# Kernel tuning notes

Hardware: AMD Instinct MI355X
Metric: run time of the kernel (lower is better)

## Reference

```python
import jax, jax.numpy as jnp
import numpy as np

HEADS = 8
DIM_HEAD = 64
DIM = 512
LN_EPS = 1e-5


def rotate_half(t):
    shp = t.shape
    t = t.reshape(*shp[:-1], -1, 2)
    t1, t2 = t[..., 0], t[..., 1]
    return jnp.stack((-t2, t1), axis=-1).reshape(shp)


def apply_rope(freqs, t):
    # freqs: (b,1,n,dh) broadcast against t: (b,h,n,dh); rot_dim == dh so no pass-through
    return t * jnp.cos(freqs) + rotate_half(t) * jnp.sin(freqs)


def layer_norm(x, g, b, eps=LN_EPS):
    mu = jnp.mean(x, axis=-1, keepdims=True)
    var = jnp.var(x, axis=-1, keepdims=True)
    return (x - mu) * jax.lax.rsqrt(var + eps) * g + b


def setup_inputs() -> dict:
    key = jax.random.key(0)
    ks = jax.random.split(key, 8)
    n, b = 2048, 4
    inner = HEADS * DIM_HEAD
    inp = {
        "x": jax.random.normal(ks[0], (n, b, DIM), dtype=jnp.float32),
        "rot_pos_emb": jax.random.uniform(ks[1], (b, n, DIM_HEAD), dtype=jnp.float32),
        "Wq": jax.random.normal(ks[2], (inner, DIM), dtype=jnp.float32) * (DIM ** -0.5),
        "Wk": jax.random.normal(ks[3], (inner, DIM), dtype=jnp.float32) * (DIM ** -0.5),
        "Wv": jax.random.normal(ks[4], (inner, DIM), dtype=jnp.float32) * (DIM ** -0.5),
        "Wo": jax.random.normal(ks[5], (DIM, inner), dtype=jnp.float32) * (inner ** -0.5),
        "bo": jnp.zeros((DIM,), dtype=jnp.float32),
        "ln_g": jnp.ones((DIM,), dtype=jnp.float32),
        "ln_b": jnp.zeros((DIM,), dtype=jnp.float32),
        "head_scale": jnp.ones((1, HEADS, 1, 1), dtype=jnp.float32),
        "ls_scale": jnp.full((1, 1, DIM), 1e-5, dtype=jnp.float32),
    }
    return inp


def reference(x, rot_pos_emb, Wq, Wk, Wv, Wo, bo, ln_g, ln_b, head_scale, ls_scale):
    n, b, d = x.shape
    h, dh = HEADS, DIM_HEAD
    scale = dh ** -0.5

    xb = jnp.transpose(x, (1, 0, 2))  # (b,n,d)
    q = (xb @ Wq.T).reshape(b, n, h, dh).transpose(0, 2, 1, 3)  # (b,h,n,dh)
    k = (xb @ Wk.T).reshape(b, n, h, dh).transpose(0, 2, 1, 3)
    v = (xb @ Wv.T).reshape(b, n, h, dh).transpose(0, 2, 1, 3)

    freqs = rot_pos_emb[:, None]  # (b,1,n,dh)
    q = apply_rope(freqs, q)
    k = apply_rope(freqs, k)

    sim = jnp.einsum("bhid,bhjd->bhij", q, k) * scale
    mask = jnp.triu(jnp.ones((n, n), dtype=bool), 1)
    sim = jnp.where(mask[None, None], -jnp.finfo(sim.dtype).max, sim)
    attn = jax.nn.softmax(sim, axis=-1)

    out = jnp.einsum("bhij,bhjd->bhid", attn, v) * head_scale
    out = out.transpose(0, 2, 1, 3).reshape(b, n, h * dh)
    out = layer_norm(out @ Wo.T + bo, ln_g, ln_b)
    out = jnp.transpose(out, (1, 0, 2))  # (n,b,d)
    return ls_scale * out
```

## Files before the change

kernel.cpp:

```cpp
#include <hip/hip_runtime.h>
#include <hip/hip_bf16.h>
#include <math.h>

#define NSEQ 2048
#define NB 4
#define NH 8
#define DH 64
#define DMODEL 512
#define MROWS (NSEQ * 4)

typedef short bf16x8 __attribute__((ext_vector_type(8)));
typedef float f32x4 __attribute__((ext_vector_type(4)));

static __device__ __forceinline__ short f2bf_r(float f) {
    unsigned u = __float_as_uint(f);
    u += 0x7FFF + ((u >> 16) & 1);
    return (short)(u >> 16);
}
static __device__ __forceinline__ unsigned bfpack(float a, float b) {
    unsigned ua = __float_as_uint(a); ua += 0x7FFF + ((ua >> 16) & 1);
    unsigned ub = __float_as_uint(b); ub += 0x7FFF + ((ub >> 16) & 1);
    return (ua >> 16) | (ub & 0xFFFF0000u);
}

__global__ __launch_bounds__(256) void k0_convert(
    const float* __restrict__ x, const float* __restrict__ Wq,
    const float* __restrict__ Wk, const float* __restrict__ Wv,
    const float* __restrict__ Wo,
    __hip_bfloat16* __restrict__ xb, __hip_bfloat16* __restrict__ Wb)
{
    const int idx = blockIdx.x * 256 + threadIdx.x;
    if (idx < 8192 * 128) {
        const int row = idx >> 7, c = (idx & 127) << 2;
        const int bi = row >> 11, ni = row & 2047;
        float4 v = *(const float4*)(x + ((size_t)(ni * NB + bi)) * DMODEL + c);
        uint2 u; u.x = bfpack(v.x, v.y); u.y = bfpack(v.z, v.w);
        *(uint2*)((short*)xb + (size_t)row * 512 + c) = u;
    } else {
        const int j = idx - 8192 * 128;
        const int row = j >> 7, c = (j & 127) << 2;
        const float* src = (row < 512) ? Wq : (row < 1024) ? Wk
                         : (row < 1536) ? Wv : Wo;
        const int rr = row & 511;
        float4 v = *(const float4*)(src + (size_t)rr * 512 + c);
        uint2 u; u.x = bfpack(v.x, v.y); u.y = bfpack(v.z, v.w);
        *(uint2*)((short*)Wb + (size_t)row * 512 + c) = u;
    }
}

__global__ __launch_bounds__(256) void k1_qkv(
    const __hip_bfloat16* __restrict__ xb, const float* __restrict__ rope,
    const __hip_bfloat16* __restrict__ Wb,
    __hip_bfloat16* __restrict__ Qs, __hip_bfloat16* __restrict__ Ks,
    __hip_bfloat16* __restrict__ Vs)
{
    __shared__ short As[128 * 72];
    __shared__ short Bs[128 * 72];
    const int t = threadIdx.x;
    const int w = t >> 6, L = t & 63, lo = L & 15, g = L >> 4;
    const int mh = (w >> 1) << 6, nh = (w & 1) << 6;

    const int lid = (int)(blockIdx.y * gridDim.x + blockIdx.x);
    const int xcd = lid & 7, slot = lid >> 3;
    const int row_blk = xcd * 8 + (slot & 7);
    const int col_blk = slot >> 3;
    const int row0 = row_blk * 128, col0 = col_blk * 128;

    f32x4 acc[4][4] = {};
    for (int k0 = 0; k0 < DMODEL; k0 += 64) {
        __syncthreads();
#pragma unroll
        for (int c = 0; c < 4; ++c) {
            const int idx = c * 256 + t;
            const int m = idx >> 3, kb = idx & 7;
            *(uint4*)&As[m * 72 + kb * 8] =
                *(const uint4*)((const short*)xb + (size_t)(row0 + m) * 512 + k0 + kb * 8);
            *(uint4*)&Bs[m * 72 + kb * 8] =
                *(const uint4*)((const short*)Wb + (size_t)(col0 + m) * 512 + k0 + kb * 8);
        }
        __syncthreads();
#pragma unroll
        for (int ks = 0; ks < 2; ++ks) {
            bf16x8 af[4], bfr[4];
#pragma unroll
            for (int mi = 0; mi < 4; ++mi)
                af[mi] = *(const bf16x8*)&As[(mh + mi * 16 + lo) * 72 + ks * 32 + g * 8];
#pragma unroll
            for (int ni = 0; ni < 4; ++ni)
                bfr[ni] = *(const bf16x8*)&Bs[(nh + ni * 16 + lo) * 72 + ks * 32 + g * 8];
#pragma unroll
            for (int mi = 0; mi < 4; ++mi)
#pragma unroll
                for (int ni = 0; ni < 4; ++ni)
                    acc[mi][ni] = __builtin_amdgcn_mfma_f32_16x16x32_bf16(
                        af[mi], bfr[ni], acc[mi][ni], 0, 0, 0);
        }
    }

    const int region = col0 >> 9;
    const int cbase = col0 & 511;
    const int bi = row0 >> 11;
    const int ni0 = row0 & 2047;
    const float SC = 0.125f * 1.44269504088896f;
    if (region < 2) {
        short* outp = (short*)((region == 0) ? Qs : Ks);
        const float qs = (region == 0) ? SC : 1.0f;
#pragma unroll
        for (int ni = 0; ni < 4; ++ni) {
            const int c = cbase + nh + ni * 16 + lo;
            const int h = c >> 6, e = c & 63;
            const float sgn = (e & 1) ? 1.0f : -1.0f;
            short* hb = outp + ((size_t)(bi * NH + h) * 128) * 1024
                        + (e >> 5) * 512 + ((e >> 3) & 3) * 16 * 8 + (e & 7);
#pragma unroll
            for (int mi = 0; mi < 4; ++mi) {
#pragma unroll
                for (int r = 0; r < 4; ++r) {
                    const int nseq = ni0 + mh + mi * 16 + g * 4 + r;
                    const float f = rope[((size_t)bi * NSEQ + nseq) * DH + e];
                    const float v = acc[mi][ni][r];
                    const float p = __shfl_xor(v, 1);
                    float sv, cv;
                    __sincosf(f, &sv, &cv);
                    const float rv = (v * cv + sgn * p * sv) * qs;
                    hb[(size_t)(nseq >> 4) * 1024 + (nseq & 15) * 8] = f2bf_r(rv);
                }
            }
        }
    } else {
#pragma unroll
        for (int ni = 0; ni < 4; ++ni) {
            const int c = cbase + nh + ni * 16 + lo;
            const int h = c >> 6, e = c & 63;
            short* hb = (short*)Vs + ((size_t)(bi * NH + h) * 256) * 512
                        + (e >> 4) * 512 + (e & 15) * 8;
#pragma unroll
            for (int mi = 0; mi < 4; ++mi) {
                const int nb = ni0 + mh + mi * 16 + g * 4;
                uint2 u;
                u.x = bfpack(acc[mi][ni][0], acc[mi][ni][1]);
                u.y = bfpack(acc[mi][ni][2], acc[mi][ni][3]);
                *(uint2*)(hb + (size_t)(nb >> 5) * 2048 + ((nb >> 3) & 3) * 16 * 8
                          + (nb & 7)) = u;
            }
        }
    }
}

__global__ __launch_bounds__(256, 3) void k2_attn(
    const __hip_bfloat16* __restrict__ Qs, const __hip_bfloat16* __restrict__ Ks,
    const __hip_bfloat16* __restrict__ Vs, const float* __restrict__ head_scale,
    __hip_bfloat16* __restrict__ Ob)
{
    __shared__ short sP[4][16 * 72];

    const int t = threadIdx.x;
    const int w = t >> 6, L = t & 63, lo = L & 15, g = L >> 4;

    const int lid = (int)blockIdx.x;
    const int xcd = lid & 7, slot = lid >> 3;
    const int bh = xcd * 4 + (slot & 3);
    const int qb = 31 - (slot >> 2);
    const int qt = qb * 4 + w;
    const int bi = bh >> 3, h = bh & 7;

    const short* Kp = (const short*)Ks + (size_t)bh * (128 * 1024) + L * 8;
    const short* Vp = (const short*)Vs + (size_t)bh * (256 * 512) + L * 8;
    const short* Qp = (const short*)Qs + (size_t)bh * (128 * 1024)
                      + (size_t)qt * 1024 + L * 8;
    const bf16x8 qf0 = *(const bf16x8*)(Qp);
    const bf16x8 qf1 = *(const bf16x8*)(Qp + 512);

    f32x4 acc[4] = {};
    float l_i = 0.f;
    const int nkt = qb + 1;

    auto body = [&](const bf16x8* kc0, const bf16x8* kc1, int kt) {
        const bool diag = (kt == qb);
        const int mlim = diag ? w : 3;
        const bool hi = (mlim >= 2);

        bf16x8 vb0[4], vb1[4];
        const short* vp0 = Vp + (size_t)(kt * 8) * 512;
#pragma unroll
        for (int dt = 0; dt < 4; ++dt) {
            vb0[dt] = *(const bf16x8*)(vp0 + dt * 512);
            if (hi) vb1[dt] = *(const bf16x8*)(vp0 + (4 + dt) * 512);
        }

        f32x4 s[4];
#pragma unroll
        for (int mt = 0; mt < 4; ++mt) {
            if (mt <= mlim) {
                f32x4 z = {};
                z = __builtin_amdgcn_mfma_f32_16x16x32_bf16(kc0[mt], qf0, z, 0, 0, 0);
                s[mt] = __builtin_amdgcn_mfma_f32_16x16x32_bf16(kc1[mt], qf1, z, 0, 0, 0);
                if (diag && mt == mlim) {
#pragma unroll
                    for (int r = 0; r < 4; ++r)
                        if ((g * 4 + r) > lo) s[mt][r] = -1e30f;
                }
            }
        }

#pragma unroll
        for (int mt = 0; mt < 4; ++mt) {
            uint2 u;
            if (mt <= mlim) {
                const float p0 = exp2f(s[mt][0] - 16.f);
                const float p1 = exp2f(s[mt][1] - 16.f);
                const float p2 = exp2f(s[mt][2] - 16.f);
                const float p3 = exp2f(s[mt][3] - 16.f);
                l_i += (p0 + p1) + (p2 + p3);
                u.x = bfpack(p0, p1); u.y = bfpack(p2, p3);
            } else {
                u.x = 0u; u.y = 0u;
            }
            *(uint2*)&sP[w][lo * 72 + mt * 16 + g * 4] = u;
        }

        const bf16x8 pb0 = *(const bf16x8*)&sP[w][lo * 72 + g * 8];
        if (hi) {
            const bf16x8 pb1 = *(const bf16x8*)&sP[w][lo * 72 + 32 + g * 8];
#pragma unroll
            for (int dt = 0; dt < 4; ++dt) {
                acc[dt] = __builtin_amdgcn_mfma_f32_16x16x32_bf16(vb0[dt], pb0, acc[dt], 0, 0, 0);
                acc[dt] = __builtin_amdgcn_mfma_f32_16x16x32_bf16(vb1[dt], pb1, acc[dt], 0, 0, 0);
            }
        } else {
#pragma unroll
            for (int dt = 0; dt < 4; ++dt)
                acc[dt] = __builtin_amdgcn_mfma_f32_16x16x32_bf16(vb0[dt], pb0, acc[dt], 0, 0, 0);
        }
    };

    bf16x8 kA0[4], kA1[4], kB0[4], kB1[4];
#pragma unroll
    for (int mt = 0; mt < 4; ++mt) {
        const short* kp = Kp + (size_t)mt * 1024;
        kA0[mt] = *(const bf16x8*)kp;
        kA1[mt] = *(const bf16x8*)(kp + 512);
    }
    int kt = 0;
#pragma unroll 1
    while (true) {
        if (kt + 1 < nkt) {
            const short* kp = Kp + (size_t)((kt + 1) * 4) * 1024;
#pragma unroll
            for (int mt = 0; mt < 4; ++mt) {
                kB0[mt] = *(const bf16x8*)(kp + mt * 1024);
                kB1[mt] = *(const bf16x8*)(kp + mt * 1024 + 512);
            }
        }
        body(kA0, kA1, kt);
        ++kt;
        if (kt >= nkt) break;
        if (kt + 1 < nkt) {
            const short* kp = Kp + (size_t)((kt + 1) * 4) * 1024;
#pragma unroll
            for (int mt = 0; mt < 4; ++mt) {
                kA0[mt] = *(const bf16x8*)(kp + mt * 1024);
                kA1[mt] = *(const bf16x8*)(kp + mt * 1024 + 512);
            }
        }
        body(kB0, kB1, kt);
        ++kt;
        if (kt >= nkt) break;
    }

    l_i += __shfl_xor(l_i, 16);
    l_i += __shfl_xor(l_i, 32);
    const float f = head_scale[h] / l_i;
    const int q = qt * 16 + lo;
    short* op = (short*)Ob + ((size_t)bi * NSEQ + q) * DMODEL + h * DH + g * 4;
#pragma unroll
    for (int dt = 0; dt < 4; ++dt) {
        uint2 u;
        u.x = bfpack(acc[dt][0] * f, acc[dt][1] * f);
        u.y = bfpack(acc[dt][2] * f, acc[dt][3] * f);
        *(uint2*)(op + dt * 16) = u;
    }
}

__global__ __launch_bounds__(256) void k3_proj(
    const __hip_bfloat16* __restrict__ Ob, const __hip_bfloat16* __restrict__ Wob,
    const float* __restrict__ bo, float* __restrict__ C2)
{
    __shared__ short As[128 * 72];
    __shared__ short Bs[128 * 72];
    const int t = threadIdx.x;
    const int w = t >> 6, L = t & 63, lo = L & 15, g = L >> 4;
    const int mh = (w >> 1) << 6, nh = (w & 1) << 6;

    const int lid = (int)(blockIdx.y * gridDim.x + blockIdx.x);
    const int xcd = lid & 7, slot = lid >> 3;
    const int row_blk = xcd * 8 + (slot & 7);
    const int col_blk = slot >> 3;
    const int row0 = row_blk * 128, col0 = col_blk * 128;

    f32x4 acc[4][4] = {};
    for (int k0 = 0; k0 < DMODEL; k0 += 64) {
        __syncthreads();
#pragma unroll
        for (int c = 0; c < 4; ++c) {
            const int idx = c * 256 + t;
            const int m = idx >> 3, kb = idx & 7;
            *(uint4*)&As[m * 72 + kb * 8] =
                *(const uint4*)((const short*)Ob + (size_t)(row0 + m) * 512 + k0 + kb * 8);
            *(uint4*)&Bs[m * 72 + kb * 8] =
                *(const uint4*)((const short*)Wob + (size_t)(col0 + m) * 512 + k0 + kb * 8);
        }
        __syncthreads();
#pragma unroll
        for (int ks = 0; ks < 2; ++ks) {
            bf16x8 af[4], bfr[4];
#pragma unroll
            for (int mi = 0; mi < 4; ++mi)
                af[mi] = *(const bf16x8*)&As[(mh + mi * 16 + lo) * 72 + ks * 32 + g * 8];
#pragma unroll
            for (int ni = 0; ni < 4; ++ni)
                bfr[ni] = *(const bf16x8*)&Bs[(nh + ni * 16 + lo) * 72 + ks * 32 + g * 8];
#pragma unroll
            for (int mi = 0; mi < 4; ++mi)
#pragma unroll
                for (int ni = 0; ni < 4; ++ni)
                    acc[mi][ni] = __builtin_amdgcn_mfma_f32_16x16x32_bf16(
                        af[mi], bfr[ni], acc[mi][ni], 0, 0, 0);
        }
    }
#pragma unroll
    for (int ni = 0; ni < 4; ++ni) {
        const int c = col0 + nh + ni * 16 + lo;
        const float b = bo[c];
#pragma unroll
        for (int mi = 0; mi < 4; ++mi) {
#pragma unroll
            for (int r = 0; r < 4; ++r) {
                const int m = row0 + mh + mi * 16 + g * 4 + r;
                C2[(size_t)m * DMODEL + c] = acc[mi][ni][r] + b;
            }
        }
    }
}

__global__ __launch_bounds__(256) void k4_ln(
    const float* __restrict__ C2, const float* __restrict__ g,
    const float* __restrict__ bln, const float* __restrict__ ls,
    float* __restrict__ out)
{
    const int m = blockIdx.x;
    const int bi = m >> 11, ni = m & (NSEQ - 1);
    const float* row = C2 + (size_t)m * DMODEL;
    const int t = threadIdx.x;
    float v0 = row[t], v1 = row[t + 256];
    float s = v0 + v1, sq2 = v0 * v0 + v1 * v1;
#pragma unroll
    for (int off = 32; off > 0; off >>= 1) {
        s += __shfl_down(s, off);
        sq2 += __shfl_down(sq2, off);
    }
    __shared__ float red[8];
    const int wid = t >> 6;
    if ((t & 63) == 0) { red[wid] = s; red[wid + 4] = sq2; }
    __syncthreads();
    s = red[0] + red[1] + red[2] + red[3];
    sq2 = red[4] + red[5] + red[6] + red[7];
    const float mean = s * (1.f / 512.f);
    const float var = sq2 * (1.f / 512.f) - mean * mean;
    const float rstd = rsqrtf(var + 1e-5f);
    float* ob = out + ((size_t)ni * NB + bi) * DMODEL;
    ob[t]       = ((v0 - mean) * rstd * g[t]       + bln[t])       * ls[t];
    ob[t + 256] = ((v1 - mean) * rstd * g[t + 256] + bln[t + 256]) * ls[t + 256];
}

extern "C" void kernel_launch(void* const* d_in, const int* in_sizes, int n_in,
                              void* d_out, int out_size, void* d_ws, size_t ws_size,
                              hipStream_t stream) {
    const float* x          = (const float*)d_in[0];
    const float* rope       = (const float*)d_in[1];
    const float* Wq         = (const float*)d_in[2];
    const float* Wk         = (const float*)d_in[3];
    const float* Wv         = (const float*)d_in[4];
    const float* Wo         = (const float*)d_in[5];
    const float* bo         = (const float*)d_in[6];
    const float* ln_g       = (const float*)d_in[7];
    const float* ln_b       = (const float*)d_in[8];
    const float* head_scale = (const float*)d_in[9];
    const float* ls_scale   = (const float*)d_in[10];
    float* out = (float*)d_out;

    char* wsb = (char*)d_ws;
    __hip_bfloat16* xb  = (__hip_bfloat16*)(wsb);
    __hip_bfloat16* Wb  = (__hip_bfloat16*)(wsb + ((size_t) 8 << 20));
    __hip_bfloat16* Qs  = (__hip_bfloat16*)(wsb + ((size_t)10 << 20));
    __hip_bfloat16* Ks  = (__hip_bfloat16*)(wsb + ((size_t)18 << 20));
    __hip_bfloat16* Vs  = (__hip_bfloat16*)(wsb + ((size_t)26 << 20));
    __hip_bfloat16* Ob  = (__hip_bfloat16*)(wsb + ((size_t)34 << 20));
    float*          C2  = (float*)(wsb + ((size_t)10 << 20));
    __hip_bfloat16* Wob = Wb + (size_t)1536 * 512;

    k0_convert<<<5120, 256, 0, stream>>>(x, Wq, Wk, Wv, Wo, xb, Wb);
    k1_qkv<<<dim3(64, 12), 256, 0, stream>>>(xb, rope, Wb, Qs, Ks, Vs);
    k2_attn<<<1024, 256, 0, stream>>>(Qs, Ks, Vs, head_scale, Ob);
    k3_proj<<<dim3(64, 4), 256, 0, stream>>>(Ob, Wob, bo, C2);
    k4_ln<<<MROWS, 256, 0, stream>>>(C2, ln_g, ln_b, ls_scale, out);
}
```

Baseline: 188.4 us.

## Precompute RoPE sin/cos and swap QK GEMM operands for vectorized epilogue

RoPE cos/sin tables are now computed once in the conversion kernel instead of per element inside the QKV epilogue. The QKV GEMM is split into a Q/K kernel and a separate V kernel. The Q/K kernel swaps its MFMA operands so each lane holds four consecutive head-dim values, which lets the rotation pair up inside a lane with no shuffle and write packed 8-byte stores. The goal is to remove the cross-lane shuffles, the repeated sincos calls and the scalar bf16 stores, at the cost of an extra kernel launch and 4 MB of cos/sin tables written and read back.

```diff
diff --git a/kernel.cpp b/kernel.cpp
--- a/kernel.cpp
+++ b/kernel.cpp
@@ -26,8 +26,9 @@
 __global__ __launch_bounds__(256) void k0_convert(
     const float* __restrict__ x, const float* __restrict__ Wq,
     const float* __restrict__ Wk, const float* __restrict__ Wv,
-    const float* __restrict__ Wo,
-    __hip_bfloat16* __restrict__ xb, __hip_bfloat16* __restrict__ Wb)
+    const float* __restrict__ Wo, const float* __restrict__ rope,
+    __hip_bfloat16* __restrict__ xb, __hip_bfloat16* __restrict__ Wb,
+    float* __restrict__ cs, float* __restrict__ sn)
 {
     const int idx = blockIdx.x * 256 + threadIdx.x;
     if (idx < 8192 * 128) {
@@ -36,7 +37,7 @@
         float4 v = *(const float4*)(x + ((size_t)(ni * NB + bi)) * DMODEL + c);
         uint2 u; u.x = bfpack(v.x, v.y); u.y = bfpack(v.z, v.w);
         *(uint2*)((short*)xb + (size_t)row * 512 + c) = u;
-    } else {
+    } else if (idx < 8192 * 128 + 2048 * 128) {
         const int j = idx - 8192 * 128;
         const int row = j >> 7, c = (j & 127) << 2;
         const float* src = (row < 512) ? Wq : (row < 1024) ? Wk
@@ -45,26 +46,37 @@
         float4 v = *(const float4*)(src + (size_t)rr * 512 + c);
         uint2 u; u.x = bfpack(v.x, v.y); u.y = bfpack(v.z, v.w);
         *(uint2*)((short*)Wb + (size_t)row * 512 + c) = u;
-    }
-}
-
-__global__ __launch_bounds__(256) void k1_qkv(
-    const __hip_bfloat16* __restrict__ xb, const float* __restrict__ rope,
-    const __hip_bfloat16* __restrict__ Wb,
-    __hip_bfloat16* __restrict__ Qs, __hip_bfloat16* __restrict__ Ks,
-    __hip_bfloat16* __restrict__ Vs)
+    } else {
+        const int j = idx - (8192 * 128 + 2048 * 128);
+        float4 f = *(const float4*)(rope + (size_t)j * 4);
+        float4 c4, s4;
+        __sincosf(f.x, &s4.x, &c4.x);
+        __sincosf(f.y, &s4.y, &c4.y);
+        __sincosf(f.z, &s4.z, &c4.z);
+        __sincosf(f.w, &s4.w, &c4.w);
+        *(float4*)(cs + (size_t)j * 4) = c4;
+        *(float4*)(sn + (size_t)j * 4) = s4;
+    }
+}
+
+__global__ __launch_bounds__(256) void k1_qk(
+    const __hip_bfloat16* __restrict__ xb, const float* __restrict__ cs,
+    const float* __restrict__ sn, const __hip_bfloat16* __restrict__ Wb,
+    __hip_bfloat16* __restrict__ Qs, __hip_bfloat16* __restrict__ Ks)
 {
     __shared__ short As[128 * 72];
     __shared__ short Bs[128 * 72];
     const int t = threadIdx.x;
     const int w = t >> 6, L = t & 63, lo = L & 15, g = L >> 4;
-    const int mh = (w >> 1) << 6, nh = (w & 1) << 6;
+    const int mhW = (w >> 1) << 6;
+    const int nhX = (w & 1) << 6;
 
     const int lid = (int)(blockIdx.y * gridDim.x + blockIdx.x);
     const int xcd = lid & 7, slot = lid >> 3;
     const int row_blk = xcd * 8 + (slot & 7);
     const int col_blk = slot >> 3;
     const int row0 = row_blk * 128, col0 = col_blk * 128;
+    const int bi = row0 >> 11, ni0 = row0 & 2047;
 
     f32x4 acc[4][4] = {};
     for (int k0 = 0; k0 < DMODEL; k0 += 64) {
@@ -84,10 +96,10 @@
             bf16x8 af[4], bfr[4];
 #pragma unroll
             for (int mi = 0; mi < 4; ++mi)
-                af[mi] = *(const bf16x8*)&As[(mh + mi * 16 + lo) * 72 + ks * 32 + g * 8];
+                af[mi] = *(const bf16x8*)&Bs[(mhW + mi * 16 + lo) * 72 + ks * 32 + g * 8];
 #pragma unroll
             for (int ni = 0; ni < 4; ++ni)
-                bfr[ni] = *(const bf16x8*)&Bs[(nh + ni * 16 + lo) * 72 + ks * 32 + g * 8];
+                bfr[ni] = *(const bf16x8*)&As[(nhX + ni * 16 + lo) * 72 + ks * 32 + g * 8];
 #pragma unroll
             for (int mi = 0; mi < 4; ++mi)
 #pragma unroll
@@ -97,52 +109,93 @@
         }
     }
 
-    const int region = col0 >> 9;
+    const float SC = 0.125f * 1.44269504088896f;
+    short* outp = (short*)((col0 < 512) ? Qs : Ks);
+    const float qs = (col0 < 512) ? SC : 1.0f;
     const int cbase = col0 & 511;
-    const int bi = row0 >> 11;
-    const int ni0 = row0 & 2047;
-    const float SC = 0.125f * 1.44269504088896f;
-    if (region < 2) {
-        short* outp = (short*)((region == 0) ? Qs : Ks);
-        const float qs = (region == 0) ? SC : 1.0f;
+#pragma unroll
+    for (int mi = 0; mi < 4; ++mi) {
+        const int c0 = cbase + mhW + mi * 16 + (g << 2);
+        const int h = c0 >> 6, e0 = c0 & 63;
+        short* hb = outp + ((size_t)(bi * NH + h)) * 131072
+                    + (e0 >> 5) * 512 + ((e0 >> 3) & 3) * 128 + (e0 & 7);
 #pragma unroll
         for (int ni = 0; ni < 4; ++ni) {
-            const int c = cbase + nh + ni * 16 + lo;
-            const int h = c >> 6, e = c & 63;
-            const float sgn = (e & 1) ? 1.0f : -1.0f;
-            short* hb = outp + ((size_t)(bi * NH + h) * 128) * 1024
-                        + (e >> 5) * 512 + ((e >> 3) & 3) * 16 * 8 + (e & 7);
-#pragma unroll
-            for (int mi = 0; mi < 4; ++mi) {
-#pragma unroll
-                for (int r = 0; r < 4; ++r) {
-                    const int nseq = ni0 + mh + mi * 16 + g * 4 + r;
-                    const float f = rope[((size_t)bi * NSEQ + nseq) * DH + e];
-                    const float v = acc[mi][ni][r];
-                    const float p = __shfl_xor(v, 1);
-                    float sv, cv;
-                    __sincosf(f, &sv, &cv);
-                    const float rv = (v * cv + sgn * p * sv) * qs;
-                    hb[(size_t)(nseq >> 4) * 1024 + (nseq & 15) * 8] = f2bf_r(rv);
-                }
-            }
-        }
-    } else {
-#pragma unroll
-        for (int ni = 0; ni < 4; ++ni) {
-            const int c = cbase + nh + ni * 16 + lo;
-            const int h = c >> 6, e = c & 63;
-            short* hb = (short*)Vs + ((size_t)(bi * NH + h) * 256) * 512
-                        + (e >> 4) * 512 + (e & 15) * 8;
-#pragma unroll
-            for (int mi = 0; mi < 4; ++mi) {
-                const int nb = ni0 + mh + mi * 16 + g * 4;
-                uint2 u;
-                u.x = bfpack(acc[mi][ni][0], acc[mi][ni][1]);
-                u.y = bfpack(acc[mi][ni][2], acc[mi][ni][3]);
-                *(uint2*)(hb + (size_t)(nb >> 5) * 2048 + ((nb >> 3) & 3) * 16 * 8
-                          + (nb & 7)) = u;
-            }
+            const int nseq = ni0 + nhX + ni * 16 + lo;
+            const float4 c4 = *(const float4*)(cs + ((size_t)bi * NSEQ + nseq) * DH + e0);
+            const float4 s4 = *(const float4*)(sn + ((size_t)bi * NSEQ + nseq) * DH + e0);
+            const f32x4 v = acc[mi][ni];
+            const float o0 = (v[0] * c4.x - v[1] * s4.x) * qs;
+            const float o1 = (v[1] * c4.y + v[0] * s4.y) * qs;
+            const float o2 = (v[2] * c4.z - v[3] * s4.z) * qs;
+            const float o3 = (v[3] * c4.w + v[2] * s4.w) * qs;
+            uint2 u; u.x = bfpack(o0, o1); u.y = bfpack(o2, o3);
+            *(uint2*)(hb + (size_t)(nseq >> 4) * 1024 + (nseq & 15) * 8) = u;
+        }
+    }
+}
+
+__global__ __launch_bounds__(256) void k1_v(
+    const __hip_bfloat16* __restrict__ xb, const __hip_bfloat16* __restrict__ Wb,
+    __hip_bfloat16* __restrict__ Vs)
+{
+    __shared__ short As[128 * 72];
+    __shared__ short Bs[128 * 72];
+    const int t = threadIdx.x;
+    const int w = t >> 6, L = t & 63, lo = L & 15, g = L >> 4;
+    const int mh = (w >> 1) << 6, nh = (w & 1) << 6;
+
+    const int lid = (int)(blockIdx.y * gridDim.x + blockIdx.x);
+    const int xcd = lid & 7, slot = lid >> 3;
+    const int row_blk = xcd * 8 + (slot & 7);
+    const int col_blk = slot >> 3;
+    const int row0 = row_blk * 128, col0 = col_blk * 128;
+    const int bi = row0 >> 11, ni0 = row0 & 2047;
+
+    f32x4 acc[4][4] = {};
+    for (int k0 = 0; k0 < DMODEL; k0 += 64) {
+        __syncthreads();
+#pragma unroll
+        for (int c = 0; c < 4; ++c) {
+            const int idx = c * 256 + t;
+            const int m = idx >> 3, kb = idx & 7;
+            *(uint4*)&As[m * 72 + kb * 8] =
+                *(const uint4*)((const short*)xb + (size_t)(row0 + m) * 512 + k0 + kb * 8);
+            *(uint4*)&Bs[m * 72 + kb * 8] =
+                *(const uint4*)((const short*)Wb + (size_t)(1024 + col0 + m) * 512 + k0 + kb * 8);
+        }
+        __syncthreads();
+#pragma unroll
+        for (int ks = 0; ks < 2; ++ks) {
+            bf16x8 af[4], bfr[4];
+#pragma unroll
+            for (int mi = 0; mi < 4; ++mi)
+                af[mi] = *(const bf16x8*)&As[(mh + mi * 16 + lo) * 72 + ks * 32 + g * 8];
+#pragma unroll
+            for (int ni = 0; ni < 4; ++ni)
+                bfr[ni] = *(const bf16x8*)&Bs[(nh + ni * 16 + lo) * 72 + ks * 32 + g * 8];
+#pragma unroll
+            for (int mi = 0; mi < 4; ++mi)
+#pragma unroll
+                for (int ni = 0; ni < 4; ++ni)
+                    acc[mi][ni] = __builtin_amdgcn_mfma_f32_16x16x32_bf16(
+                        af[mi], bfr[ni], acc[mi][ni], 0, 0, 0);
+        }
+    }
+#pragma unroll
+    for (int ni = 0; ni < 4; ++ni) {
+        const int c = col0 + nh + ni * 16 + lo;
+        const int h = c >> 6, e = c & 63;
+        short* hb = (short*)Vs + ((size_t)(bi * NH + h)) * 131072
+                    + (e >> 4) * 512 + (e & 15) * 8;
+#pragma unroll
+        for (int mi = 0; mi < 4; ++mi) {
+            const int nb = ni0 + mh + mi * 16 + g * 4;
+            uint2 u;
+            u.x = bfpack(acc[mi][ni][0], acc[mi][ni][1]);
+            u.y = bfpack(acc[mi][ni][2], acc[mi][ni][3]);
+            *(uint2*)(hb + (size_t)(nb >> 5) * 2048 + ((nb >> 3) & 3) * 128
+                      + (nb & 7)) = u;
         }
     }
 }
@@ -396,11 +449,14 @@
     __hip_bfloat16* Ks  = (__hip_bfloat16*)(wsb + ((size_t)18 << 20));
     __hip_bfloat16* Vs  = (__hip_bfloat16*)(wsb + ((size_t)26 << 20));
     __hip_bfloat16* Ob  = (__hip_bfloat16*)(wsb + ((size_t)34 << 20));
+    float*          cs  = (float*)(wsb + ((size_t)42 << 20));
+    float*          sn  = (float*)(wsb + ((size_t)44 << 20));
     float*          C2  = (float*)(wsb + ((size_t)10 << 20));
     __hip_bfloat16* Wob = Wb + (size_t)1536 * 512;
 
-    k0_convert<<<5120, 256, 0, stream>>>(x, Wq, Wk, Wv, Wo, xb, Wb);
-    k1_qkv<<<dim3(64, 12), 256, 0, stream>>>(xb, rope, Wb, Qs, Ks, Vs);
+    k0_convert<<<5632, 256, 0, stream>>>(x, Wq, Wk, Wv, Wo, rope, xb, Wb, cs, sn);
+    k1_qk<<<dim3(64, 8), 256, 0, stream>>>(xb, cs, sn, Wb, Qs, Ks);
+    k1_v<<<dim3(64, 4), 256, 0, stream>>>(xb, Wb, Vs);
     k2_attn<<<1024, 256, 0, stream>>>(Qs, Ks, Vs, head_scale, Ob);
     k3_proj<<<dim3(64, 4), 256, 0, stream>>>(Ob, Wob, bo, C2);
     k4_ln<<<MROWS, 256, 0, stream>>>(C2, ln_g, ln_b, ls_scale, out);
```

After: 194.2 us. +3.1%, slower.
